# Kernel optimization log

Measured on AMD Instinct MI355X. Metric: run time of the kernel, lower is better.

The kernel has to match this reference:

```python
import jax, jax.numpy as jnp
import numpy as np

K = 20  # neighbors (includes self, as PyG knn(x,x,k) does)
B, P = 8, 2048


def _knn_idx(pts, k):
    # pts: [P, D] -> [P, k] indices of k nearest (self included, dist 0)
    sq = jnp.sum(pts * pts, axis=-1)
    dist = sq[:, None] + sq[None, :] - 2.0 * (pts @ pts.T)
    return jax.lax.top_k(-dist, k)[1]


def _edge_conv(x, W, b, k):
    # DynamicEdgeConv with single-Linear nn and max aggregation.
    # x: [B,P,D]; W: [C, 2D]; message = Lin([x_i, x_j - x_i])
    D = x.shape[-1]
    Wa, Wb = W[:, :D], W[:, D:]
    idx = jax.vmap(lambda p: _knn_idx(p, k))(x)                 # [B,P,k]
    nb = jax.vmap(lambda xb, ib: xb[ib])(x, idx)                # [B,P,k,D]
    msg = (x @ Wa.T)[:, :, None, :] + (nb - x[:, :, None, :]) @ Wb.T + b
    return jnp.max(msg, axis=2)                                 # [B,P,C]


def _lin(h, W, b):
    return h @ W.T + b


def setup_inputs() -> dict:
    key = jax.random.key(0)
    ks = jax.random.split(key, 16)
    N = B * P

    def w(k_, shape):
        fan_in = shape[-1]
        return (jax.random.normal(k_, shape, dtype=jnp.float32) / np.sqrt(fan_in)).astype(jnp.float32)

    inp = {
        "pos": jax.random.normal(ks[0], (N, 3), dtype=jnp.float32),
        "x": jax.random.normal(ks[1], (N, 3), dtype=jnp.float32),
        "features": jax.random.normal(ks[2], (N, 1344), dtype=jnp.float32),
        "batch": (jnp.arange(N) // P).astype(jnp.int64) if jax.config.jax_enable_x64 else (jnp.arange(N) // P).astype(jnp.int32),
        # filter_conv: Conv2d(1344,128,1) == Linear 1344->128
        "Wf": w(ks[3], (128, 1344)), "bf": jnp.zeros((128,), jnp.float32),
        # edge MLPs (single Linear each, plain_last)
        "W1": w(ks[4], (64, 2 * 134)), "b1": jnp.zeros((64,), jnp.float32),
        "W2": w(ks[5], (128, 2 * 64)), "b2": jnp.zeros((128,), jnp.float32),
        "W3": w(ks[6], (256, 2 * 128)), "b3": jnp.zeros((256,), jnp.float32),
        # fc1: Linear 576->1024
        "Wfc1": w(ks[7], (1024, 576)), "bfc1": jnp.zeros((1024,), jnp.float32),
        # fc2: 1024->512->256->23 with ReLU on hidden layers
        "Wfa": w(ks[8], (512, 1024)), "bfa": jnp.zeros((512,), jnp.float32),
        "Wfb": w(ks[9], (256, 512)), "bfb": jnp.zeros((256,), jnp.float32),
        "Wfc": w(ks[10], (23, 256)), "bfc": jnp.zeros((23,), jnp.float32),
    }
    return inp


def reference(pos, x, features, batch, Wf, bf, W1, b1, W2, b2, W3, b3,
              Wfc1, bfc1, Wfa, bfa, Wfb, bfb, Wfc, bfc):
    N = pos.shape[0]
    nB = int(batch[-1]) + 1
    nP = N // nB

    feats = _lin(features, Wf, bf)                              # [N,128] (1x1 conv)
    h0 = jnp.concatenate([pos, x, feats], axis=1).reshape(nB, nP, -1)  # [B,P,134]

    x1 = _edge_conv(h0, W1, b1, K)                              # [B,P,64]
    x2 = _edge_conv(x1, W2, b2, K)                              # [B,P,128]
    x3 = _edge_conv(x2, W3, b3, K)                              # [B,P,256]

    cat = jnp.concatenate([x1, x2, x3, feats.reshape(nB, nP, -1)], axis=-1)  # [B,P,576]
    h = _lin(cat, Wfc1, bfc1)                                   # [B,P,1024]
    g = jnp.max(h, axis=1)                                      # global_max_pool -> [B,1024]
    g = jax.nn.relu(_lin(g, Wfa, bfa))
    g = jax.nn.relu(_lin(g, Wfb, bfb))
    g = _lin(g, Wfc, bfc)
    return jax.nn.log_softmax(g, axis=1)                        # [B,23]
```

## Files before the change

kernel.cpp:

```cpp
#include <hip/hip_runtime.h>
#include <math.h>

#define PPB 2048
#define NBATCH 8
#define KNN 20

typedef __attribute__((ext_vector_type(8))) short short8;
typedef __attribute__((ext_vector_type(8))) __bf16 bf16x8;
typedef __attribute__((ext_vector_type(4))) float f32x4;

__global__ __launch_bounds__(256) void gemm_feats_kernel(
    const float* __restrict__ X, const float* __restrict__ W,
    float* __restrict__ fpart, int N) {
  const int KC = 336;
  int kc = blockIdx.z;
  const float* Xp = X + kc * KC;
  const float* Wp = W + kc * KC;
  float* Y = fpart + (size_t)kc * N * 128;
  __shared__ float Xs[8][132];
  __shared__ float Ws[8][132];
  int t = threadIdx.x;
  int tx = t & 15, ty = t >> 4;
  int i0 = blockIdx.y * 128;
  float acc[8][8];
#pragma unroll
  for (int r = 0; r < 8; ++r)
#pragma unroll
    for (int n = 0; n < 8; ++n) acc[r][n] = 0.f;

  for (int k0 = 0; k0 < KC; k0 += 8) {
#pragma unroll
    for (int p = 0; p < 4; ++p) {
      int e = t + p * 256, r = e >> 3, c = e & 7, k = k0 + c;
      Xs[c][r] = Xp[(size_t)(i0 + r) * 1344 + k];
      Ws[c][r] = Wp[(size_t)r * 1344 + k];
    }
    __syncthreads();
#pragma unroll
    for (int k = 0; k < 8; ++k) {
      float4 a0 = *(const float4*)&Xs[k][ty * 8];
      float4 a1 = *(const float4*)&Xs[k][ty * 8 + 4];
      float a[8] = {a0.x, a0.y, a0.z, a0.w, a1.x, a1.y, a1.z, a1.w};
      float4 b0 = *(const float4*)&Ws[k][tx * 8];
      float4 b1 = *(const float4*)&Ws[k][tx * 8 + 4];
      float bb[8] = {b0.x, b0.y, b0.z, b0.w, b1.x, b1.y, b1.z, b1.w};
#pragma unroll
      for (int r = 0; r < 8; ++r)
#pragma unroll
        for (int n = 0; n < 8; ++n) acc[r][n] += a[r] * bb[n];
    }
    __syncthreads();
  }
#pragma unroll
  for (int r = 0; r < 8; ++r) {
    size_t row = (size_t)(i0 + ty * 8 + r) * 128 + tx * 8;
#pragma unroll
    for (int n4 = 0; n4 < 2; ++n4) {
      float4 o;
      o.x = acc[r][n4 * 4 + 0]; o.y = acc[r][n4 * 4 + 1];
      o.z = acc[r][n4 * 4 + 2]; o.w = acc[r][n4 * 4 + 3];
      *(float4*)&Y[row + n4 * 4] = o;
    }
  }
}

__global__ __launch_bounds__(256) void reduce_feats_kernel(
    const float* __restrict__ fpart, const float* __restrict__ bias,
    float* __restrict__ catbuf, int N) {
  int e = blockIdx.x * 256 + threadIdx.x;
  size_t NP = (size_t)N * 128;
  int i = e >> 7, m = e & 127;
  float s = bias[m] + fpart[e] + fpart[NP + e] + fpart[2 * NP + e] + fpart[3 * NP + e];
  catbuf[(size_t)i * 576 + 448 + m] = s;
}

__global__ __launch_bounds__(256) void feats_mfma_kernel(
    const unsigned short* __restrict__ Xh, const unsigned short* __restrict__ Xl,
    const unsigned short* __restrict__ Wh, const unsigned short* __restrict__ Wl,
    const float* __restrict__ bias, float* __restrict__ catbuf) {
  __shared__ unsigned short XsH[64][40], XsL[64][40];
  __shared__ unsigned short WsH[64][40], WsL[64][40];
  int t = threadIdx.x;
  int l = t & 63, w = t >> 6;
  int i0 = blockIdx.y * 64, m0 = blockIdx.x * 64;
  int r_st = t >> 2, c_st = (t & 3) * 8;

  f32x4 acc[4];
#pragma unroll
  for (int g = 0; g < 4; ++g) acc[g] = (f32x4){0.f, 0.f, 0.f, 0.f};

  for (int k0 = 0; k0 < 1344; k0 += 32) {
    short8 xh = *(const short8*)&Xh[(size_t)(i0 + r_st) * 1344 + k0 + c_st];
    short8 xl = *(const short8*)&Xl[(size_t)(i0 + r_st) * 1344 + k0 + c_st];
    short8 wh = *(const short8*)&Wh[(size_t)(m0 + r_st) * 1344 + k0 + c_st];
    short8 wl = *(const short8*)&Wl[(size_t)(m0 + r_st) * 1344 + k0 + c_st];
    __syncthreads();
    *(short8*)&XsH[r_st][c_st] = xh;
    *(short8*)&XsL[r_st][c_st] = xl;
    *(short8*)&WsH[r_st][c_st] = wh;
    *(short8*)&WsL[r_st][c_st] = wl;
    __syncthreads();
    bf16x8 ah = __builtin_bit_cast(bf16x8, *(const short8*)&XsH[16 * w + (l & 15)][(l >> 4) * 8]);
    bf16x8 al = __builtin_bit_cast(bf16x8, *(const short8*)&XsL[16 * w + (l & 15)][(l >> 4) * 8]);
#pragma unroll
    for (int g = 0; g < 4; ++g) {
      bf16x8 bh = __builtin_bit_cast(bf16x8, *(const short8*)&WsH[g * 16 + (l & 15)][(l >> 4) * 8]);
      bf16x8 bl = __builtin_bit_cast(bf16x8, *(const short8*)&WsL[g * 16 + (l & 15)][(l >> 4) * 8]);
      acc[g] = __builtin_amdgcn_mfma_f32_16x16x32_bf16(ah, bh, acc[g], 0, 0, 0);
      acc[g] = __builtin_amdgcn_mfma_f32_16x16x32_bf16(ah, bl, acc[g], 0, 0, 0);
      acc[g] = __builtin_amdgcn_mfma_f32_16x16x32_bf16(al, bh, acc[g], 0, 0, 0);
    }
  }
  int qr = (l >> 4) * 4;
#pragma unroll
  for (int g = 0; g < 4; ++g) {
    int col = m0 + g * 16 + (l & 15);
    float bv = bias[col];
#pragma unroll
    for (int r = 0; r < 4; ++r) {
      int row = i0 + w * 16 + qr + r;
      catbuf[(size_t)row * 576 + 448 + col] = acc[g][r] + bv;
    }
  }
}

__global__ __launch_bounds__(256) void edge_gemm_kernel(
    const float* __restrict__ X, int ldx, int D,
    const float* __restrict__ W, int ldw, int M,
    float* __restrict__ A, float* __restrict__ Pb) {
  __shared__ float Xs[16][68];
  __shared__ float Ws[16][68];
  int t = threadIdx.x, tx = t & 15, ty = t >> 4;
  int nHalf = M >> 6;
  int mt = blockIdx.x;
  int is_b = (mt >= nHalf) ? 1 : 0;
  int m0 = (is_b ? mt - nHalf : mt) << 6;
  int koff = is_b ? D : 0;
  float* __restrict__ out = is_b ? Pb : A;
  int i0 = blockIdx.y * 64;
  float acc[4][4];
#pragma unroll
  for (int r = 0; r < 4; ++r)
#pragma unroll
    for (int n = 0; n < 4; ++n) acc[r][n] = 0.f;

  for (int k0 = 0; k0 < D; k0 += 16) {
#pragma unroll
    for (int p = 0; p < 4; ++p) {
      int e = t + p * 256, r = e >> 4, c = e & 15, k = k0 + c;
      Xs[c][r] = (k < D) ? X[(size_t)(i0 + r) * ldx + k] : 0.f;
      Ws[c][r] = (k < D) ? W[(size_t)(m0 + r) * ldw + koff + k] : 0.f;
    }
    __syncthreads();
#pragma unroll
    for (int kk = 0; kk < 16; ++kk) {
      float4 a4 = *(const float4*)&Xs[kk][ty * 4];
      float4 b4 = *(const float4*)&Ws[kk][tx * 4];
      float a[4] = {a4.x, a4.y, a4.z, a4.w};
      float bb[4] = {b4.x, b4.y, b4.z, b4.w};
#pragma unroll
      for (int r = 0; r < 4; ++r)
#pragma unroll
        for (int n = 0; n < 4; ++n) acc[r][n] += a[r] * bb[n];
    }
    __syncthreads();
  }
#pragma unroll
  for (int r = 0; r < 4; ++r) {
    float4 o;
    o.x = acc[r][0]; o.y = acc[r][1]; o.z = acc[r][2]; o.w = acc[r][3];
    *(float4*)&out[(size_t)(i0 + ty * 4 + r) * M + m0 + tx * 4] = o;
  }
}

__global__ __launch_bounds__(256) void cast_bf16_kernel(
    const float* __restrict__ src, unsigned short* __restrict__ dst, int n) {
  int e4 = (blockIdx.x * 256 + threadIdx.x) * 4;
  if (e4 >= n) return;
  float4 v = *(const float4*)&src[e4];
  ushort4 o;
  unsigned int u;
  u = __float_as_uint(v.x); o.x = (unsigned short)((u + 0x7fff + ((u >> 16) & 1)) >> 16);
  u = __float_as_uint(v.y); o.y = (unsigned short)((u + 0x7fff + ((u >> 16) & 1)) >> 16);
  u = __float_as_uint(v.z); o.z = (unsigned short)((u + 0x7fff + ((u >> 16) & 1)) >> 16);
  u = __float_as_uint(v.w); o.w = (unsigned short)((u + 0x7fff + ((u >> 16) & 1)) >> 16);
  *(ushort4*)&dst[e4] = o;
}

__global__ __launch_bounds__(256) void cast_hl_kernel(
    const float* __restrict__ X, int ldx, int D, int Kp,
    unsigned short* __restrict__ hi, unsigned short* __restrict__ lo,
    float* __restrict__ sq) {
  __shared__ float red[256];
  int i = blockIdx.x;
  int t = threadIdx.x;
  float s = 0.f;
  for (int k = t; k < Kp; k += 256) {
    float x = (k < D) ? X[(size_t)i * ldx + k] : 0.f;
    unsigned int u = __float_as_uint(x);
    unsigned short h = (unsigned short)((u + 0x7fff + ((u >> 16) & 1)) >> 16);
    float hf = __uint_as_float((unsigned int)h << 16);
    float r = x - hf;
    unsigned int v = __float_as_uint(r);
    unsigned short l16 = (unsigned short)((v + 0x7fff + ((v >> 16) & 1)) >> 16);
    hi[(size_t)i * Kp + k] = h;
    lo[(size_t)i * Kp + k] = l16;
    s += x * x;
  }
  red[t] = s;
  __syncthreads();
  for (int off = 128; off > 0; off >>= 1) {
    if (t < off) red[t] += red[t + off];
    __syncthreads();
  }
  if (t == 0) sq[i] = red[0];
}

template <int KP>
__global__ __launch_bounds__(256) void dist_gemm2_kernel(
    const unsigned short* __restrict__ Xhi,
    const unsigned short* __restrict__ Xlo,
    const float* __restrict__ sq,
    float* __restrict__ dist, int zBase) {
  __shared__ unsigned short Ah[128][40];
  __shared__ unsigned short Al[128][40];
  __shared__ unsigned short Bh[64][40];
  __shared__ unsigned short Bl[64][40];
  int t = threadIdx.x;
  int l = t & 63, w = t >> 6;
  int z = blockIdx.z;
  size_t bbase = (size_t)(zBase + z) * PPB;
  int c0 = blockIdx.x * 64, q0 = blockIdx.y * 128;

  f32x4 acc[2][4];
#pragma unroll
  for (int qs = 0; qs < 2; ++qs)
#pragma unroll
    for (int cc = 0; cc < 4; ++cc) acc[qs][cc] = (f32x4){0.f, 0.f, 0.f, 0.f};

  for (int k0 = 0; k0 < KP; k0 += 32) {
    short8 sa[2][2];
#pragma unroll
    for (int p = 0; p < 2; ++p) {
      int e = t + p * 256, row = e >> 2, kg = e & 3;
      sa[p][0] = *(const short8*)&Xhi[(bbase + q0 + row) * KP + k0 + kg * 8];
      sa[p][1] = *(const short8*)&Xlo[(bbase + q0 + row) * KP + k0 + kg * 8];
    }
    int brow = t >> 2, bkg = t & 3;
    short8 sb0 = *(const short8*)&Xhi[(bbase + c0 + brow) * KP + k0 + bkg * 8];
    short8 sb1 = *(const short8*)&Xlo[(bbase + c0 + brow) * KP + k0 + bkg * 8];
    __syncthreads();
#pragma unroll
    for (int p = 0; p < 2; ++p) {
      int e = t + p * 256, row = e >> 2, kg = e & 3;
      *(short8*)&Ah[row][kg * 8] = sa[p][0];
      *(short8*)&Al[row][kg * 8] = sa[p][1];
    }
    *(short8*)&Bh[brow][bkg * 8] = sb0;
    *(short8*)&Bl[brow][bkg * 8] = sb1;
    __syncthreads();

    bf16x8 ah[2], al[2], bh[4], bl[4];
#pragma unroll
    for (int qs = 0; qs < 2; ++qs) {
      int row = w * 32 + qs * 16 + (l & 15);
      ah[qs] = __builtin_bit_cast(bf16x8, *(const short8*)&Ah[row][(l >> 4) * 8]);
      al[qs] = __builtin_bit_cast(bf16x8, *(const short8*)&Al[row][(l >> 4) * 8]);
    }
#pragma unroll
    for (int cc = 0; cc < 4; ++cc) {
      bh[cc] = __builtin_bit_cast(bf16x8, *(const short8*)&Bh[cc * 16 + (l & 15)][(l >> 4) * 8]);
      bl[cc] = __builtin_bit_cast(bf16x8, *(const short8*)&Bl[cc * 16 + (l & 15)][(l >> 4) * 8]);
    }
#pragma unroll
    for (int qs = 0; qs < 2; ++qs)
#pragma unroll
      for (int cc = 0; cc < 4; ++cc) {
        acc[qs][cc] = __builtin_amdgcn_mfma_f32_16x16x32_bf16(ah[qs], bh[cc], acc[qs][cc], 0, 0, 0);
        acc[qs][cc] = __builtin_amdgcn_mfma_f32_16x16x32_bf16(ah[qs], bl[cc], acc[qs][cc], 0, 0, 0);
        acc[qs][cc] = __builtin_amdgcn_mfma_f32_16x16x32_bf16(al[qs], bh[cc], acc[qs][cc], 0, 0, 0);
      }
  }
  float* dz = dist + (size_t)z * PPB * PPB;
#pragma unroll
  for (int cc = 0; cc < 4; ++cc) {
    int j = c0 + cc * 16 + (l & 15);
    float sqj = sq[bbase + j];
#pragma unroll
    for (int qs = 0; qs < 2; ++qs) {
      int qb = q0 + w * 32 + qs * 16 + (l >> 4) * 4;
#pragma unroll
      for (int r = 0; r < 4; ++r)
        dz[(size_t)(qb + r) * PPB + j] = sqj - 2.f * acc[qs][cc][r];
    }
  }
}

__global__ __launch_bounds__(256) void knn_sel3_kernel(
    const float* __restrict__ dist, int zBase, int* __restrict__ idx) {
  int z = blockIdx.y;
  int b = zBase + z;
  int q = blockIdx.x * 4 + (threadIdx.x >> 6);
  int lane = threadIdx.x & 63;
  const float* row = dist + ((size_t)z * PPB + q) * PPB + lane * 32;

  float v[32];
#pragma unroll
  for (int m4 = 0; m4 < 8; ++m4) {
    float4 f = *(const float4*)&row[m4 * 4];
    v[m4 * 4 + 0] = f.x; v[m4 * 4 + 1] = f.y;
    v[m4 * 4 + 2] = f.z; v[m4 * 4 + 3] = f.w;
  }
  float gv[8]; int gi[8];
#pragma unroll
  for (int g = 0; g < 8; ++g) {
    float bv = v[g * 4]; int bi = 0;
    if (v[g * 4 + 1] < bv) { bv = v[g * 4 + 1]; bi = 1; }
    if (v[g * 4 + 2] < bv) { bv = v[g * 4 + 2]; bi = 2; }
    if (v[g * 4 + 3] < bv) { bv = v[g * 4 + 3]; bi = 3; }
    gv[g] = bv; gi[g] = g * 4 + bi;
  }
  float lv = gv[0]; int lm = gi[0];
#pragma unroll
  for (int g = 1; g < 8; ++g)
    if (gv[g] < lv) { lv = gv[g]; lm = gi[g]; }
  unsigned u0 = __float_as_uint(lv);
  unsigned lk = u0 ^ (((int)u0 >> 31) | 0x80000000u);

  unsigned rm = 0;
#pragma unroll
  for (int s = 0; s < KNN; ++s) {
    unsigned bk = lk;
    int bj = lane * 32 + lm;
#pragma unroll
    for (int o = 1; o < 64; o <<= 1) {
      unsigned ok = __shfl_xor(bk, o);
      int oj = __shfl_xor(bj, o);
      if (ok < bk || (ok == bk && oj < bj)) { bk = ok; bj = oj; }
    }
    if (lane == 0)
      idx[((size_t)b * PPB + q) * KNN + s] = b * PPB + bj;
    if ((bj >> 5) == lane) {
      int m = bj & 31;
      rm |= (1u << m);
      int g = m >> 2;
      float e0 = v[0], e1 = v[1], e2 = v[2], e3 = v[3];
#pragma unroll
      for (int gg = 1; gg < 8; ++gg) {
        bool sel = (g == gg);
        e0 = sel ? v[gg * 4 + 0] : e0;
        e1 = sel ? v[gg * 4 + 1] : e1;
        e2 = sel ? v[gg * 4 + 2] : e2;
        e3 = sel ? v[gg * 4 + 3] : e3;
      }
      unsigned gm = (rm >> (g * 4)) & 15u;
      if (gm & 1u) e0 = 1e38f;
      if (gm & 2u) e1 = 1e38f;
      if (gm & 4u) e2 = 1e38f;
      if (gm & 8u) e3 = 1e38f;
      float nv = e0; int ni = 0;
      if (e1 < nv) { nv = e1; ni = 1; }
      if (e2 < nv) { nv = e2; ni = 2; }
      if (e3 < nv) { nv = e3; ni = 3; }
#pragma unroll
      for (int gg = 0; gg < 8; ++gg)
        if (g == gg) { gv[gg] = nv; gi[gg] = gg * 4 + ni; }
      lv = gv[0]; lm = gi[0];
#pragma unroll
      for (int gg = 1; gg < 8; ++gg)
        if (gv[gg] < lv) { lv = gv[gg]; lm = gi[gg]; }
      unsigned u = __float_as_uint(lv);
      lk = u ^ (((int)u >> 31) | 0x80000000u);
    }
  }
}

__global__ __launch_bounds__(256) void fc1max_mfma_kernel(
    const unsigned short* __restrict__ Xb, const unsigned short* __restrict__ Wb,
    const float* __restrict__ bias, float* __restrict__ partial) {
  __shared__ unsigned short Xs[64][40];
  __shared__ unsigned short Ws[64][40];
  __shared__ float red[4][64];
  int t = threadIdx.x;
  int l = t & 63, w = t >> 6;
  int b = blockIdx.z, pt = blockIdx.y;
  int i0 = b * PPB + pt * 64;
  int m0 = blockIdx.x * 64;
  int r_st = t >> 2;
  int c_st = (t & 3) * 8;

  f32x4 acc[4];
#pragma unroll
  for (int g = 0; g < 4; ++g) acc[g] = (f32x4){0.f, 0.f, 0.f, 0.f};

  for (int k0 = 0; k0 < 576; k0 += 32) {
    short8 xv = *(const short8*)&Xb[(size_t)(i0 + r_st) * 576 + k0 + c_st];
    short8 wv = *(const short8*)&Wb[(size_t)(m0 + r_st) * 576 + k0 + c_st];
    __syncthreads();
    *(short8*)&Xs[r_st][c_st] = xv;
    *(short8*)&Ws[r_st][c_st] = wv;
    __syncthreads();
    short8 ar = *(const short8*)&Xs[16 * w + (l & 15)][(l >> 4) * 8];
    bf16x8 av = __builtin_bit_cast(bf16x8, ar);
#pragma unroll
    for (int g = 0; g < 4; ++g) {
      short8 br = *(const short8*)&Ws[g * 16 + (l & 15)][(l >> 4) * 8];
      bf16x8 bv = __builtin_bit_cast(bf16x8, br);
      acc[g] = __builtin_amdgcn_mfma_f32_16x16x32_bf16(av, bv, acc[g], 0, 0, 0);
    }
  }
  float pm[4];
#pragma unroll
  for (int g = 0; g < 4; ++g) {
    float m = fmaxf(fmaxf(acc[g][0], acc[g][1]), fmaxf(acc[g][2], acc[g][3]));
    m = fmaxf(m, __shfl_xor(m, 16));
    m = fmaxf(m, __shfl_xor(m, 32));
    pm[g] = m;
  }
  if (l < 16) {
#pragma unroll
    for (int g = 0; g < 4; ++g) red[w][g * 16 + l] = pm[g];
  }
  __syncthreads();
  if (t < 64) {
    float mx = fmaxf(fmaxf(red[0][t], red[1][t]), fmaxf(red[2][t], red[3][t]));
    partial[((size_t)b * (PPB / 64) + pt) * 1024 + m0 + t] = mx + bias[m0 + t];
  }
}

__global__ __launch_bounds__(256) void gmax_kernel(
    const float* __restrict__ partial, float* __restrict__ g) {
  int b = blockIdx.y;
  int m = blockIdx.x * 256 + threadIdx.x;
  float mx = -INFINITY;
  for (int pt = 0; pt < PPB / 64; ++pt)
    mx = fmaxf(mx, partial[((size_t)b * (PPB / 64) + pt) * 1024 + m]);
  g[b * 1024 + m] = mx;
}

__global__ __launch_bounds__(192) void h0_kernel(
    const float* __restrict__ pos, const float* __restrict__ xin,
    const float* __restrict__ catbuf, float* __restrict__ h0) {
  int i = blockIdx.x;
  int d = threadIdx.x;
  if (d < 3)        h0[(size_t)i * 134 + d] = pos[i * 3 + d];
  else if (d < 6)   h0[(size_t)i * 134 + d] = xin[i * 3 + d - 3];
  else if (d < 134) h0[(size_t)i * 134 + d] = catbuf[(size_t)i * 576 + 448 + (d - 6)];
}

__global__ __launch_bounds__(256) void edge_out_kernel(
    const float* __restrict__ A, const float* __restrict__ Pb, int M,
    const float* __restrict__ bias, const int* __restrict__ idx,
    float* __restrict__ Y, int ldy) {
  int i = blockIdx.x;
  int t = threadIdx.x;
  __shared__ int nbs[KNN];
  if (t < KNN) nbs[t] = idx[(size_t)i * KNN + t];
  __syncthreads();
  for (int m = t; m < M; m += 256) {
    float mx = -INFINITY;
#pragma unroll
    for (int kk = 0; kk < KNN; ++kk)
      mx = fmaxf(mx, Pb[(size_t)nbs[kk] * M + m]);
    Y[(size_t)i * ldy + m] = A[(size_t)i * M + m] + bias[m] - Pb[(size_t)i * M + m] + mx;
  }
}

__global__ __launch_bounds__(256) void mlp2_kernel(
    const float* __restrict__ X, const float* __restrict__ W,
    const float* __restrict__ bias, float* __restrict__ Y,
    int D, int M, int do_relu) {
  int b = blockIdx.y;
  int m = blockIdx.x * 4 + (threadIdx.x >> 6);
  int lane = threadIdx.x & 63;
  const float* xr = X + (size_t)b * D;
  const float* wr = W + (size_t)m * D;
  float s = 0.f;
  for (int k = lane * 4; k < D; k += 256) {
    float4 xv = *(const float4*)&xr[k];
    float4 wv = *(const float4*)&wr[k];
    s += xv.x * wv.x + xv.y * wv.y + xv.z * wv.z + xv.w * wv.w;
  }
#pragma unroll
  for (int o = 32; o > 0; o >>= 1) s += __shfl_down(s, o);
  if (lane == 0) {
    s += bias[m];
    if (do_relu) s = fmaxf(s, 0.f);
    Y[(size_t)b * M + m] = s;
  }
}

__global__ __launch_bounds__(256) void final2_kernel(
    const float* __restrict__ X, const float* __restrict__ W,
    const float* __restrict__ bias, float* __restrict__ out) {
  int b = blockIdx.x;
  int w = threadIdx.x >> 6, lane = threadIdx.x & 63;
  __shared__ float lg[23];
  const float* xr = X + (size_t)b * 256;
  float4 xv = *(const float4*)&xr[lane * 4];
  for (int c = w; c < 23; c += 4) {
    const float* wr = W + (size_t)c * 256;
    float4 wv = *(const float4*)&wr[lane * 4];
    float s = xv.x * wv.x + xv.y * wv.y + xv.z * wv.z + xv.w * wv.w;
#pragma unroll
    for (int o = 32; o > 0; o >>= 1) s += __shfl_down(s, o);
    if (lane == 0) lg[c] = s + bias[c];
  }
  __syncthreads();
  if (threadIdx.x == 0) {
    float mx = lg[0];
    for (int c = 1; c < 23; ++c) mx = fmaxf(mx, lg[c]);
    float s = 0.f;
    for (int c = 0; c < 23; ++c) s += expf(lg[c] - mx);
    float lse = mx + logf(s);
    for (int c = 0; c < 23; ++c) out[b * 23 + c] = lg[c] - lse;
  }
}


extern "C" void kernel_launch(void* const* d_in, const int* in_sizes, int n_in,
                              void* d_out, int out_size, void* d_ws, size_t ws_size,
                              hipStream_t stream) {
  const float* pos      = (const float*)d_in[0];
  const float* xin      = (const float*)d_in[1];
  const float* features = (const float*)d_in[2];
  const float* Wf   = (const float*)d_in[4];
  const float* bf   = (const float*)d_in[5];
  const float* W1   = (const float*)d_in[6];
  const float* b1   = (const float*)d_in[7];
  const float* W2   = (const float*)d_in[8];
  const float* b2   = (const float*)d_in[9];
  const float* W3   = (const float*)d_in[10];
  const float* b3   = (const float*)d_in[11];
  const float* Wfc1 = (const float*)d_in[12];
  const float* bfc1 = (const float*)d_in[13];
  const float* Wfa  = (const float*)d_in[14];
  const float* bfa  = (const float*)d_in[15];
  const float* Wfb  = (const float*)d_in[16];
  const float* bfb  = (const float*)d_in[17];
  const float* Wfc  = (const float*)d_in[18];
  const float* bfc  = (const float*)d_in[19];
  float* out = (float*)d_out;

  const int N = in_sizes[0] / 3;

  char* base = (char*)d_ws;
  size_t off = 0;
  auto alloc = [&](size_t bytes) {
    void* p = base + off;
    off += (bytes + 255) & ~(size_t)255;
    return p;
  };
  float* catbuf  = (float*)alloc((size_t)N * 576 * 4);
  float* h0      = (float*)alloc((size_t)N * 134 * 4);
  float* Abuf    = (float*)alloc((size_t)N * 256 * 4);
  float* Pbbuf   = (float*)alloc((size_t)N * 256 * 4);
  unsigned short* Xhi = (unsigned short*)alloc((size_t)N * 160 * 2);
  unsigned short* Xlo = (unsigned short*)alloc((size_t)N * 160 * 2);
  float* sqbuf   = (float*)alloc((size_t)N * 4);
  int*   idxbuf  = (int*)  alloc((size_t)N * KNN * 4);
  float* partial = (float*)alloc((size_t)NBATCH * (PPB / 64) * 1024 * 4);
  float* g       = (float*)alloc((size_t)NBATCH * 1024 * 4);
  float* ga      = (float*)alloc((size_t)NBATCH * 512 * 4);
  float* gb      = (float*)alloc((size_t)NBATCH * 256 * 4);

  const size_t distBatch = (size_t)PPB * PPB * 4;
  int nz;
  float* dist;
  if (ws_size >= off + 8 * distBatch + 256) {
    nz = 8;  dist = (float*)alloc(8 * distBatch);
  } else if (ws_size >= off + 4 * distBatch + 256) {
    nz = 4;  dist = (float*)alloc(4 * distBatch);
  } else {
    nz = 2;  dist = Abuf;
  }

  float* fpart = Abuf;
  unsigned short* catb16 = (unsigned short*)Abuf;
  unsigned short* Wb16   = (unsigned short*)h0;

  if (nz == 8) {
    unsigned short* featHi = (unsigned short*)dist;
    unsigned short* featLo = featHi + (size_t)N * 1344;
    unsigned short* WfHi   = (unsigned short*)partial;
    unsigned short* WfLo   = WfHi + (size_t)128 * 1344;
    cast_hl_kernel<<<N, 256, 0, stream>>>(features, 1344, 1344, 1344,
                                          featHi, featLo, sqbuf);
    cast_hl_kernel<<<128, 256, 0, stream>>>(Wf, 1344, 1344, 1344,
                                            WfHi, WfLo, sqbuf);
    feats_mfma_kernel<<<dim3(2, N / 64), 256, 0, stream>>>(
        featHi, featLo, WfHi, WfLo, bf, catbuf);
  } else {
    gemm_feats_kernel<<<dim3(1, N / 128, 4), 256, 0, stream>>>(features, Wf, fpart, N);
    reduce_feats_kernel<<<(N * 128) / 256, 256, 0, stream>>>(fpart, bf, catbuf, N);
  }

  h0_kernel<<<N, 192, 0, stream>>>(pos, xin, catbuf, h0);

  struct Layer {
    const float* Xin; int ldx; int D; int Kp;
    const float* W; int ldw;
    const float* bias; int M;
    float* Yout;
  };
  Layer L[3] = {
      {h0,          134, 134, 160, W1, 268, b1,  64, catbuf + 0},
      {catbuf + 0,  576,  64,  64, W2, 128, b2, 128, catbuf + 64},
      {catbuf + 64, 576, 128, 128, W3, 256, b3, 256, catbuf + 192},
  };

  for (int l = 0; l < 3; ++l) {
    cast_hl_kernel<<<N, 256, 0, stream>>>(L[l].Xin, L[l].ldx, L[l].D, L[l].Kp,
                                          Xhi, Xlo, sqbuf);
    for (int p = 0; p < NBATCH; p += nz) {
      if (L[l].Kp == 160)
        dist_gemm2_kernel<160><<<dim3(PPB / 64, PPB / 128, nz), 256, 0, stream>>>(
            Xhi, Xlo, sqbuf, dist, p);
      else if (L[l].Kp == 64)
        dist_gemm2_kernel<64><<<dim3(PPB / 64, PPB / 128, nz), 256, 0, stream>>>(
            Xhi, Xlo, sqbuf, dist, p);
      else
        dist_gemm2_kernel<128><<<dim3(PPB / 64, PPB / 128, nz), 256, 0, stream>>>(
            Xhi, Xlo, sqbuf, dist, p);
      knn_sel3_kernel<<<dim3(PPB / 4, nz), 256, 0, stream>>>(dist, p, idxbuf);
    }
    edge_gemm_kernel<<<dim3((2 * L[l].M) / 64, N / 64), 256, 0, stream>>>(
        L[l].Xin, L[l].ldx, L[l].D, L[l].W, L[l].ldw, L[l].M, Abuf, Pbbuf);
    edge_out_kernel<<<N, 256, 0, stream>>>(
        Abuf, Pbbuf, L[l].M, L[l].bias, idxbuf, L[l].Yout, 576);
  }

  cast_bf16_kernel<<<(N * 576) / 1024, 256, 0, stream>>>(catbuf, catb16, N * 576);
  cast_bf16_kernel<<<(1024 * 576) / 1024, 256, 0, stream>>>(Wfc1, Wb16, 1024 * 576);

  fc1max_mfma_kernel<<<dim3(1024 / 64, PPB / 64, NBATCH), 256, 0, stream>>>(
      catb16, Wb16, bfc1, partial);
  gmax_kernel<<<dim3(1024 / 256, NBATCH), 256, 0, stream>>>(partial, g);

  mlp2_kernel<<<dim3(512 / 4, NBATCH), 256, 0, stream>>>(g,  Wfa, bfa, ga, 1024, 512, 1);
  mlp2_kernel<<<dim3(256 / 4, NBATCH), 256, 0, stream>>>(ga, Wfb, bfb, gb, 512, 256, 1);
  final2_kernel<<<NBATCH, 256, 0, stream>>>(gb, Wfc, bfc, out);
}
```

Baseline: 693.8 us.

## Fuse per-32-column minima into distance GEMM epilogue, lazy rescan in kNN select

The distance GEMM epilogue now computes, for each row and each 32-column group, a packed (key,index) minimum via 16-lane shuffles and writes it to a new minbuf. The selection kernel starts from these precomputed minima instead of loading the full 2048-float row into registers. It rereads only the 32 floats of the winning group from global memory after each pick. This removes the full dist row read from the select kernel, at the cost of extra shuffles and writes in the GEMM epilogue, plus dependent global reads inside the 20-step loop.

```diff
diff --git a/kernel.cpp b/kernel.cpp
--- a/kernel.cpp
+++ b/kernel.cpp
@@ -217,11 +217,12 @@
 }
 
 template <int KP>
-__global__ __launch_bounds__(256) void dist_gemm2_kernel(
+__global__ __launch_bounds__(256) void dist_gemm3_kernel(
     const unsigned short* __restrict__ Xhi,
     const unsigned short* __restrict__ Xlo,
     const float* __restrict__ sq,
-    float* __restrict__ dist, int zBase) {
+    float* __restrict__ dist,
+    unsigned long long* __restrict__ minbuf, int zBase) {
   __shared__ unsigned short Ah[128][40];
   __shared__ unsigned short Al[128][40];
   __shared__ unsigned short Bh[64][40];
@@ -282,95 +283,84 @@
       }
   }
   float* dz = dist + (size_t)z * PPB * PPB;
-#pragma unroll
-  for (int cc = 0; cc < 4; ++cc) {
-    int j = c0 + cc * 16 + (l & 15);
-    float sqj = sq[bbase + j];
-#pragma unroll
-    for (int qs = 0; qs < 2; ++qs) {
-      int qb = q0 + w * 32 + qs * 16 + (l >> 4) * 4;
-#pragma unroll
-      for (int r = 0; r < 4; ++r)
-        dz[(size_t)(qb + r) * PPB + j] = sqj - 2.f * acc[qs][cc][r];
-    }
-  }
-}
-
-__global__ __launch_bounds__(256) void knn_sel3_kernel(
-    const float* __restrict__ dist, int zBase, int* __restrict__ idx) {
+  unsigned long long* mb = minbuf + (size_t)z * PPB * 64;
+  float sqjv[4];
+#pragma unroll
+  for (int cc = 0; cc < 4; ++cc)
+    sqjv[cc] = sq[bbase + c0 + cc * 16 + (l & 15)];
+#pragma unroll
+  for (int qs = 0; qs < 2; ++qs)
+#pragma unroll
+    for (int r = 0; r < 4; ++r) {
+      int row = q0 + w * 32 + qs * 16 + (l >> 4) * 4 + r;
+      float d[4];
+#pragma unroll
+      for (int cc = 0; cc < 4; ++cc) {
+        d[cc] = sqjv[cc] - 2.f * acc[qs][cc][r];
+        dz[(size_t)row * PPB + c0 + cc * 16 + (l & 15)] = d[cc];
+      }
+#pragma unroll
+      for (int gh = 0; gh < 2; ++gh) {
+        float v0 = d[gh * 2 + 0], v1 = d[gh * 2 + 1];
+        int cA = c0 + (gh * 2 + 0) * 16 + (l & 15);
+        int cB = c0 + (gh * 2 + 1) * 16 + (l & 15);
+        float mv = v0; int mc = cA;
+        if (v1 < mv) { mv = v1; mc = cB; }
+        unsigned u = __float_as_uint(mv);
+        unsigned k = u ^ (((int)u >> 31) | 0x80000000u);
+        unsigned long long p = ((unsigned long long)k << 32) | (unsigned)mc;
+#pragma unroll
+        for (int o = 1; o < 16; o <<= 1) {
+          unsigned long long q2 = __shfl_xor(p, o);
+          if (q2 < p) p = q2;
+        }
+        if ((l & 15) == 0)
+          mb[(size_t)row * 64 + (c0 >> 5) + gh] = p;
+      }
+    }
+}
+
+__global__ __launch_bounds__(256) void knn_sel5_kernel(
+    const float* __restrict__ dist,
+    const unsigned long long* __restrict__ minbuf,
+    int zBase, int* __restrict__ idx) {
   int z = blockIdx.y;
   int b = zBase + z;
   int q = blockIdx.x * 4 + (threadIdx.x >> 6);
-  int lane = threadIdx.x & 63;
-  const float* row = dist + ((size_t)z * PPB + q) * PPB + lane * 32;
-
-  float v[32];
-#pragma unroll
-  for (int m4 = 0; m4 < 8; ++m4) {
-    float4 f = *(const float4*)&row[m4 * 4];
-    v[m4 * 4 + 0] = f.x; v[m4 * 4 + 1] = f.y;
-    v[m4 * 4 + 2] = f.z; v[m4 * 4 + 3] = f.w;
-  }
-  float gv[8]; int gi[8];
-#pragma unroll
-  for (int g = 0; g < 8; ++g) {
-    float bv = v[g * 4]; int bi = 0;
-    if (v[g * 4 + 1] < bv) { bv = v[g * 4 + 1]; bi = 1; }
-    if (v[g * 4 + 2] < bv) { bv = v[g * 4 + 2]; bi = 2; }
-    if (v[g * 4 + 3] < bv) { bv = v[g * 4 + 3]; bi = 3; }
-    gv[g] = bv; gi[g] = g * 4 + bi;
-  }
-  float lv = gv[0]; int lm = gi[0];
-#pragma unroll
-  for (int g = 1; g < 8; ++g)
-    if (gv[g] < lv) { lv = gv[g]; lm = gi[g]; }
-  unsigned u0 = __float_as_uint(lv);
-  unsigned lk = u0 ^ (((int)u0 >> 31) | 0x80000000u);
-
+  int l = threadIdx.x & 63;
+  const float* drow = dist + ((size_t)z * PPB + q) * PPB;
+  unsigned long long P = minbuf[((size_t)z * PPB + q) * 64 + l];
   unsigned rm = 0;
 #pragma unroll
   for (int s = 0; s < KNN; ++s) {
-    unsigned bk = lk;
-    int bj = lane * 32 + lm;
+    unsigned long long p = P;
 #pragma unroll
     for (int o = 1; o < 64; o <<= 1) {
-      unsigned ok = __shfl_xor(bk, o);
-      int oj = __shfl_xor(bj, o);
-      if (ok < bk || (ok == bk && oj < bj)) { bk = ok; bj = oj; }
-    }
-    if (lane == 0)
-      idx[((size_t)b * PPB + q) * KNN + s] = b * PPB + bj;
-    if ((bj >> 5) == lane) {
-      int m = bj & 31;
-      rm |= (1u << m);
-      int g = m >> 2;
-      float e0 = v[0], e1 = v[1], e2 = v[2], e3 = v[3];
-#pragma unroll
-      for (int gg = 1; gg < 8; ++gg) {
-        bool sel = (g == gg);
-        e0 = sel ? v[gg * 4 + 0] : e0;
-        e1 = sel ? v[gg * 4 + 1] : e1;
-        e2 = sel ? v[gg * 4 + 2] : e2;
-        e3 = sel ? v[gg * 4 + 3] : e3;
+      unsigned long long t2 = __shfl_xor(p, o);
+      if (t2 < p) p = t2;
+    }
+    unsigned j = (unsigned)p;
+    if (l == 0)
+      idx[((size_t)b * PPB + q) * KNN + s] = b * PPB + (int)j;
+    if ((j >> 5) == (unsigned)l) {
+      rm |= 1u << (j & 31u);
+      const float* gp = drow + l * 32;
+      float mv = 1e38f; int mc = 0;
+#pragma unroll
+      for (int m4 = 0; m4 < 8; ++m4) {
+        float4 f = *(const float4*)&gp[m4 * 4];
+        float e0 = ((rm >> (m4 * 4 + 0)) & 1u) ? 1e38f : f.x;
+        float e1 = ((rm >> (m4 * 4 + 1)) & 1u) ? 1e38f : f.y;
+        float e2 = ((rm >> (m4 * 4 + 2)) & 1u) ? 1e38f : f.z;
+        float e3 = ((rm >> (m4 * 4 + 3)) & 1u) ? 1e38f : f.w;
+        if (e0 < mv) { mv = e0; mc = m4 * 4 + 0; }
+        if (e1 < mv) { mv = e1; mc = m4 * 4 + 1; }
+        if (e2 < mv) { mv = e2; mc = m4 * 4 + 2; }
+        if (e3 < mv) { mv = e3; mc = m4 * 4 + 3; }
       }
-      unsigned gm = (rm >> (g * 4)) & 15u;
-      if (gm & 1u) e0 = 1e38f;
-      if (gm & 2u) e1 = 1e38f;
-      if (gm & 4u) e2 = 1e38f;
-      if (gm & 8u) e3 = 1e38f;
-      float nv = e0; int ni = 0;
-      if (e1 < nv) { nv = e1; ni = 1; }
-      if (e2 < nv) { nv = e2; ni = 2; }
-      if (e3 < nv) { nv = e3; ni = 3; }
-#pragma unroll
-      for (int gg = 0; gg < 8; ++gg)
-        if (g == gg) { gv[gg] = nv; gi[gg] = gg * 4 + ni; }
-      lv = gv[0]; lm = gi[0];
-#pragma unroll
-      for (int gg = 1; gg < 8; ++gg)
-        if (gv[gg] < lv) { lv = gv[gg]; lm = gi[gg]; }
-      unsigned u = __float_as_uint(lv);
-      lk = u ^ (((int)u >> 31) | 0x80000000u);
+      unsigned u = __float_as_uint(mv);
+      unsigned k = u ^ (((int)u >> 31) | 0x80000000u);
+      P = ((unsigned long long)k << 32) | (unsigned)(l * 32 + mc);
     }
   }
 }
@@ -559,6 +549,8 @@
   unsigned short* Xlo = (unsigned short*)alloc((size_t)N * 160 * 2);
   float* sqbuf   = (float*)alloc((size_t)N * 4);
   int*   idxbuf  = (int*)  alloc((size_t)N * KNN * 4);
+  unsigned long long* minbuf =
+      (unsigned long long*)alloc((size_t)NBATCH * PPB * 64 * 8);
   float* partial = (float*)alloc((size_t)NBATCH * (PPB / 64) * 1024 * 4);
   float* g       = (float*)alloc((size_t)NBATCH * 1024 * 4);
   float* ga      = (float*)alloc((size_t)NBATCH * 512 * 4);
@@ -614,15 +606,16 @@
                                           Xhi, Xlo, sqbuf);
     for (int p = 0; p < NBATCH; p += nz) {
       if (L[l].Kp == 160)
-        dist_gemm2_kernel<160><<<dim3(PPB / 64, PPB / 128, nz), 256, 0, stream>>>(
-            Xhi, Xlo, sqbuf, dist, p);
+        dist_gemm3_kernel<160><<<dim3(PPB / 64, PPB / 128, nz), 256, 0, stream>>>(
+            Xhi, Xlo, sqbuf, dist, minbuf, p);
       else if (L[l].Kp == 64)
-        dist_gemm2_kernel<64><<<dim3(PPB / 64, PPB / 128, nz), 256, 0, stream>>>(
-            Xhi, Xlo, sqbuf, dist, p);
+        dist_gemm3_kernel<64><<<dim3(PPB / 64, PPB / 128, nz), 256, 0, stream>>>(
+            Xhi, Xlo, sqbuf, dist, minbuf, p);
       else
-        dist_gemm2_kernel<128><<<dim3(PPB / 64, PPB / 128, nz), 256, 0, stream>>>(
-            Xhi, Xlo, sqbuf, dist, p);
-      knn_sel3_kernel<<<dim3(PPB / 4, nz), 256, 0, stream>>>(dist, p, idxbuf);
+        dist_gemm3_kernel<128><<<dim3(PPB / 64, PPB / 128, nz), 256, 0, stream>>>(
+            Xhi, Xlo, sqbuf, dist, minbuf, p);
+      knn_sel5_kernel<<<dim3(PPB / 4, nz), 256, 0, stream>>>(
+          dist, minbuf, p, idxbuf);
     }
     edge_gemm_kernel<<<dim3((2 * L[l].M) / 64, N / 64), 256, 0, stream>>>(
         L[l].Xin, L[l].ldx, L[l].D, L[l].W, L[l].ldw, L[l].M, Abuf, Pbbuf);
```

New measurement: 858.2 us. +23.7%, slower.
